# Performance work log

Measured on AMD Instinct MI355X. Metric: run time of the kernel, lower is better.

The kernel has to match this reference:

```python
import jax, jax.numpy as jnp
import numpy as np

N_NODES = 50000
N_EDGES = 800000
D_IN = 128
D_HID = 128
D_OUT = 128


def _glorot(key, shape):
    fan_in, fan_out = shape
    lim = np.sqrt(6.0 / (fan_in + fan_out))
    return jax.random.uniform(key, shape, jnp.float32, -lim, lim)


def setup_inputs() -> dict:
    key = jax.random.key(0)
    ks = jax.random.split(key, 8)
    x = jax.random.normal(ks[0], (N_NODES, D_IN), jnp.float32)
    edge_index = jax.random.randint(ks[1], (2, N_EDGES), 0, N_NODES, jnp.int64)
    # SAGEConv layer 1: lin_l (neighbor aggregate, has bias), lin_r (root, no bias)
    W1l = _glorot(ks[2], (D_IN, D_HID))
    b1 = jnp.zeros((D_HID,), jnp.float32)
    W1r = _glorot(ks[3], (D_IN, D_HID))
    # SAGEConv layer 2
    W2l = _glorot(ks[4], (D_HID, D_OUT))
    b2 = jnp.zeros((D_OUT,), jnp.float32)
    W2r = _glorot(ks[5], (D_HID, D_OUT))
    return {"x": x, "edge_index": edge_index, "W1l": W1l, "b1": b1,
            "W1r": W1r, "W2l": W2l, "b2": b2, "W2r": W2r}


def _sage_conv(x, src, dst, Wl, bl, Wr):
    # mean-aggregate neighbor features j -> i, then out = mean @ Wl + b + x @ Wr
    msg_sum = jax.ops.segment_sum(x[src], dst, num_segments=N_NODES)  # [N, F]
    cnt = jax.ops.segment_sum(jnp.ones((src.shape[0],), x.dtype), dst,
                              num_segments=N_NODES)  # [N]
    mean = msg_sum / jnp.maximum(cnt, 1.0)[:, None]
    return mean @ Wl + bl + x @ Wr


def reference(x, edge_index, W1l, b1, W1r, W2l, b2, W2r):
    src, dst = edge_index[0], edge_index[1]
    h = _sage_conv(x, src, dst, W1l, b1, W1r)
    h = jax.nn.relu(h)
    # dropout(p=0.2) is identity in eval mode
    out = _sage_conv(h, src, dst, W2l, b2, W2r)
    return out
```

## Files before the change

### kernel.cpp

```cpp
#include <hip/hip_runtime.h>

#define N_NODES 50000
#define N_EDGES 800000
#define D 128
#define CAP 64
#define NPB 512
#define NBIN 98
#define BIN_CAP 12288
#define EPB 4096

typedef __attribute__((ext_vector_type(8))) short s16x8;
typedef __attribute__((ext_vector_type(8))) unsigned short u16x8;
typedef __attribute__((ext_vector_type(4))) unsigned short u16x4;
typedef __attribute__((ext_vector_type(4))) float f32x4;

__device__ __forceinline__ unsigned short f2bf(float f) {
    unsigned u = __builtin_bit_cast(unsigned, f);
    return (unsigned short)((u + 0x7FFFu + ((u >> 16) & 1u)) >> 16);
}
__device__ __forceinline__ float bf2f(unsigned short h) {
    return __builtin_bit_cast(float, (unsigned)h << 16);
}

__device__ __forceinline__ int load_src(const int* ei, int is32, int e) {
    return is32 ? ei[e] : ei[2 * e];
}
__device__ __forceinline__ int load_dst(const int* ei, int is32, int e) {
    return is32 ? ei[N_EDGES + e] : ei[2 * N_EDGES + 2 * e];
}

__global__ void prep_kernel(const float* __restrict__ x, const int* __restrict__ ei,
                            const float* __restrict__ W1l, const float* __restrict__ W1r,
                            const float* __restrict__ W2l, const float* __restrict__ W2r,
                            unsigned short* __restrict__ xb,
                            unsigned short* __restrict__ wt1,
                            unsigned short* __restrict__ wt2,
                            int* __restrict__ flag, int* __restrict__ bin_cnt) {
    int b = blockIdx.x;
    if (b < 3125) {
        int t = b * 256 + threadIdx.x;
        float4 a = *(const float4*)(x + (size_t)t * 8);
        float4 c = *(const float4*)(x + (size_t)t * 8 + 4);
        u16x8 o;
        o[0] = f2bf(a.x); o[1] = f2bf(a.y); o[2] = f2bf(a.z); o[3] = f2bf(a.w);
        o[4] = f2bf(c.x); o[5] = f2bf(c.y); o[6] = f2bf(c.z); o[7] = f2bf(c.w);
        *(u16x8*)(xb + (size_t)t * 8) = o;
    } else if (b < 3381) {
        int idx = b - 3125;
        int layer = idx >> 7;
        int c = idx & 127;
        int k = threadIdx.x;
        const float* Wl = layer ? W2l : W1l;
        const float* Wr = layer ? W2r : W1r;
        unsigned short* wt = layer ? wt2 : wt1;
        float v = (k < 128) ? Wl[(size_t)k * 128 + c] : Wr[(size_t)(k - 128) * 128 + c];
        wt[c * 256 + k] = f2bf(v);
    } else {
        if (threadIdx.x < 128) bin_cnt[threadIdx.x] = 0;
        __shared__ int any;
        if (threadIdx.x == 0) any = 0;
        __syncthreads();
        if (ei[2 * threadIdx.x + 1] != 0) atomicOr(&any, 1);
        __syncthreads();
        if (threadIdx.x == 0) flag[0] = any;
    }
}

__global__ __launch_bounds__(256) void binp_kernel(const int* __restrict__ ei,
                                                   const int* __restrict__ flag,
                                                   int* __restrict__ bin_cnt,
                                                   unsigned* __restrict__ bins) {
    __shared__ unsigned sBuf[EPB];
    __shared__ int bcnt[128], brun[128], bpos[128], gbase[128];
    int tid = threadIdx.x;
    int blk = blockIdx.x;
    int e0 = blk * EPB + tid * 16;
    int nblk = N_EDGES - blk * EPB;
    if (nblk > EPB) nblk = EPB;
    bool valid = (tid * 16) < nblk;
    if (tid < 128) bcnt[tid] = 0;
    __syncthreads();
    unsigned packed[16];
    if (valid) {
        int is32 = flag[0];
        if (is32) {
            const int4* ps = (const int4*)(ei + e0);
            const int4* pd = (const int4*)(ei + N_EDGES + e0);
#pragma unroll
            for (int q = 0; q < 4; ++q) {
                int4 s = ps[q], d = pd[q];
                packed[q * 4 + 0] = ((unsigned)d.x << 16) | (unsigned)s.x;
                packed[q * 4 + 1] = ((unsigned)d.y << 16) | (unsigned)s.y;
                packed[q * 4 + 2] = ((unsigned)d.z << 16) | (unsigned)s.z;
                packed[q * 4 + 3] = ((unsigned)d.w << 16) | (unsigned)s.w;
            }
        } else {
            const int4* ps = (const int4*)(ei + 2 * (size_t)e0);
            const int4* pd = (const int4*)(ei + 2 * (size_t)N_EDGES + 2 * (size_t)e0);
#pragma unroll
            for (int q = 0; q < 8; ++q) {
                int4 s = ps[q], d = pd[q];
                packed[q * 2 + 0] = ((unsigned)d.x << 16) | (unsigned)s.x;
                packed[q * 2 + 1] = ((unsigned)d.z << 16) | (unsigned)s.z;
            }
        }
#pragma unroll
        for (int k = 0; k < 16; ++k) atomicAdd(&bcnt[packed[k] >> 25], 1);
    }
    __syncthreads();
    if (tid < 64) {
        int a = bcnt[2 * tid], b = bcnt[2 * tid + 1];
        int s = a + b;
        int incl = s;
#pragma unroll
        for (int o = 1; o < 64; o <<= 1) {
            int t = __shfl_up(incl, o, 64);
            if (tid >= o) incl += t;
        }
        int pref = incl - s;
        brun[2 * tid] = pref;
        brun[2 * tid + 1] = pref + a;
        bpos[2 * tid] = pref;
        bpos[2 * tid + 1] = pref + a;
    }
    __syncthreads();
    if (valid) {
#pragma unroll
        for (int k = 0; k < 16; ++k) {
            int b = packed[k] >> 25;
            int slot = atomicAdd(&bpos[b], 1);
            sBuf[slot] = packed[k];
        }
    }
    __syncthreads();
    if (tid < 128) {
        int n = bcnt[tid];
        gbase[tid] = n > 0 ? atomicAdd(&bin_cnt[tid], n) : 0;
    }
    __syncthreads();
    for (int i = tid; i < nblk; i += 256) {
        unsigned p = sBuf[i];
        int b = p >> 25;
        int gpos = gbase[b] + (i - brun[b]);
        if (gpos < BIN_CAP) bins[(size_t)b * BIN_CAP + gpos] = p;
    }
}

__global__ __launch_bounds__(256) void unbin_kernel(const int* __restrict__ bin_cnt,
                                                    const unsigned* __restrict__ bins,
                                                    int* __restrict__ cnt,
                                                    unsigned short* __restrict__ srcs16) {
    __shared__ unsigned short buck[NPB * CAP];
    __shared__ int lcnt[NPB];
    int tid = threadIdx.x;
    int bn = blockIdx.x;
    int nbase = bn * NPB;
    for (int i = tid; i < NPB; i += 256) lcnt[i] = 0;
    __syncthreads();
    int nE = bin_cnt[bn];
    if (nE > BIN_CAP) nE = BIN_CAP;
    for (int i = tid; i < nE; i += 256) {
        unsigned p = bins[(size_t)bn * BIN_CAP + i];
        int local = (int)(p >> 16) - nbase;
        if ((unsigned)local < NPB) {
            int slot = atomicAdd(&lcnt[local], 1);
            if (slot < CAP) buck[local * CAP + slot] = (unsigned short)(p & 0xFFFFu);
        }
    }
    __syncthreads();
    int nlim = N_NODES - nbase;
    if (nlim > NPB) nlim = NPB;
    const uint4* sb = (const uint4*)buck;
    uint4* go = (uint4*)(srcs16 + (size_t)nbase * CAP);
    int n4 = nlim * 8;
    for (int i = tid; i < n4; i += 256) go[i] = sb[i];
    for (int i = tid; i < nlim; i += 256) cnt[nbase + i] = lcnt[i];
}

__global__ __launch_bounds__(256) void aggp_kernel(const unsigned short* __restrict__ feat,
                                                   const int* __restrict__ cnt,
                                                   const unsigned short* __restrict__ srcs16,
                                                   unsigned short* __restrict__ agg) {
    int node = blockIdx.x * 4 + (threadIdx.x >> 6);
    if (node >= N_NODES) return;
    int lane = threadIdx.x & 63;
    int q = lane >> 4;
    int c16 = lane & 15;
    int deg = cnt[node];
    int idx = srcs16[node * CAP + lane];
    int d = deg < CAP ? deg : CAP;
    float acc[8] = {};
    for (int j = 0; j < d; j += 16) {
        int e[4];
        float m[4];
#pragma unroll
        for (int u = 0; u < 4; ++u) {
            int jj = j + u * 4 + q;
            int es = __shfl(idx, jj, 64);
            bool val = jj < d;
            e[u] = val ? es : 0;
            m[u] = val ? 1.f : 0.f;
        }
        u16x8 v[4];
#pragma unroll
        for (int u = 0; u < 4; ++u)
            v[u] = *((const u16x8*)(feat + (size_t)e[u] * D) + c16);
#pragma unroll
        for (int u = 0; u < 4; ++u)
#pragma unroll
            for (int i = 0; i < 8; ++i)
                acc[i] += bf2f((unsigned short)v[u][i]) * m[u];
    }
#pragma unroll
    for (int i = 0; i < 8; ++i) {
        acc[i] += __shfl_xor(acc[i], 16, 64);
        acc[i] += __shfl_xor(acc[i], 32, 64);
    }
    if (q == 0) {
        float s = deg > 0 ? 1.f / (float)deg : 0.f;
        u16x8 o;
#pragma unroll
        for (int i = 0; i < 8; ++i) o[i] = f2bf(acc[i] * s);
        *((u16x8*)(agg + (size_t)node * D) + c16) = o;
    }
}

template <int MODE>
__global__ __launch_bounds__(256) void mm3_kernel(const unsigned short* __restrict__ Agb,
                                                  const unsigned short* __restrict__ Rootb,
                                                  const unsigned short* __restrict__ Wt,
                                                  const float* __restrict__ bias,
                                                  float* __restrict__ C,
                                                  unsigned short* __restrict__ Cb) {
    __shared__ __align__(16) unsigned short sA[2][32][128];
    int r0 = blockIdx.x * 32;
    int tid = threadIdx.x;
    int lane = tid & 63, wid = tid >> 6;
    int l15 = lane & 15, khalf = lane >> 4;

    s16x8 bF[2][4][2];
#pragma unroll
    for (int p = 0; p < 2; ++p)
#pragma unroll
        for (int kc2 = 0; kc2 < 4; ++kc2)
#pragma unroll
            for (int nf = 0; nf < 2; ++nf) {
                int cc = wid * 32 + nf * 16 + l15;
                bF[p][kc2][nf] = *(const s16x8*)(Wt + (size_t)cc * 256 + p * 128 +
                                                 kc2 * 32 + khalf * 8);
            }

    {
        int r = tid >> 3;
        int kq = tid & 7;
        int row = r0 + r;
        u16x8 a0, a1, x0, x1;
        if (row < N_NODES) {
            const u16x8* pa = (const u16x8*)(Agb + (size_t)row * D + kq * 16);
            a0 = pa[0]; a1 = pa[1];
            const u16x8* pr = (const u16x8*)(Rootb + (size_t)row * D + kq * 16);
            x0 = pr[0]; x1 = pr[1];
        } else {
            u16x8 z = {};
            a0 = z; a1 = z; x0 = z; x1 = z;
        }
        int c0 = (kq * 2) ^ (r & 7), c1 = (kq * 2 + 1) ^ (r & 7);
        *(u16x8*)&sA[0][r][c0 * 8] = a0;
        *(u16x8*)&sA[0][r][c1 * 8] = a1;
        *(u16x8*)&sA[1][r][c0 * 8] = x0;
        *(u16x8*)&sA[1][r][c1 * 8] = x1;
    }
    __syncthreads();

    f32x4 acc[2][2] = {};
#pragma unroll
    for (int p = 0; p < 2; ++p)
#pragma unroll
        for (int kc2 = 0; kc2 < 4; ++kc2) {
            s16x8 aF[2];
#pragma unroll
            for (int mf = 0; mf < 2; ++mf) {
                int rr = mf * 16 + l15;
                int chunk = (kc2 * 4 + khalf) ^ (rr & 7);
                aF[mf] = *(const s16x8*)&sA[p][rr][chunk * 8];
            }
#pragma unroll
            for (int nf = 0; nf < 2; ++nf)
#pragma unroll
                for (int mf = 0; mf < 2; ++mf)
                    acc[mf][nf] = __builtin_amdgcn_mfma_f32_16x16x32_bf16(
                        aF[mf], bF[p][kc2][nf], acc[mf][nf], 0, 0, 0);
        }

#pragma unroll
    for (int mf = 0; mf < 2; ++mf)
#pragma unroll
        for (int nf = 0; nf < 2; ++nf) {
            int col = wid * 32 + nf * 16 + l15;
            float b = bias[col];
#pragma unroll
            for (int r = 0; r < 4; ++r) {
                int row = r0 + mf * 16 + khalf * 4 + r;
                if (row < N_NODES) {
                    float o = acc[mf][nf][r] + b;
                    if (MODE == 1) {
                        o = fmaxf(o, 0.f);
                        Cb[(size_t)row * D + col] = f2bf(o);
                    } else {
                        C[(size_t)row * D + col] = o;
                    }
                }
            }
        }
}

__global__ void initc_kernel(const int* __restrict__ ei, int* __restrict__ flag,
                             int* __restrict__ cnt) {
    int i = blockIdx.x * 256 + threadIdx.x;
    if (i < 50048) cnt[i] = 0;
    if (blockIdx.x == 0) {
        __shared__ int any;
        if (threadIdx.x == 0) any = 0;
        __syncthreads();
        if (ei[2 * threadIdx.x + 1] != 0) atomicOr(&any, 1);
        __syncthreads();
        if (threadIdx.x == 0) flag[0] = any;
    }
}

__global__ void prep_wf_kernel(const float* __restrict__ W1l, const float* __restrict__ W1r,
                               const float* __restrict__ W2l, const float* __restrict__ W2r,
                               unsigned short* __restrict__ wt1,
                               unsigned short* __restrict__ wt2) {
    int layer = blockIdx.x >> 7;
    int c = blockIdx.x & 127;
    int k = threadIdx.x;
    const float* Wl = layer ? W2l : W1l;
    const float* Wr = layer ? W2r : W1r;
    unsigned short* wt = layer ? wt2 : wt1;
    float v = (k < 128) ? Wl[(size_t)k * 128 + c] : Wr[(size_t)(k - 128) * 128 + c];
    wt[c * 256 + k] = f2bf(v);
}

__global__ void tobf_kernel(const float* __restrict__ in, unsigned short* __restrict__ out,
                            int n8) {
    int t = blockIdx.x * 256 + threadIdx.x;
    if (t >= n8) return;
    float4 a = *(const float4*)(in + (size_t)t * 8);
    float4 b = *(const float4*)(in + (size_t)t * 8 + 4);
    u16x8 o;
    o[0] = f2bf(a.x); o[1] = f2bf(a.y); o[2] = f2bf(a.z); o[3] = f2bf(a.w);
    o[4] = f2bf(b.x); o[5] = f2bf(b.y); o[6] = f2bf(b.z); o[7] = f2bf(b.w);
    *(u16x8*)(out + (size_t)t * 8) = o;
}

__global__ void hist_kernel(const int* __restrict__ ei, const int* __restrict__ flag,
                            int* __restrict__ cnt) {
    int e = blockIdx.x * blockDim.x + threadIdx.x;
    if (e >= N_EDGES) return;
    int is32 = flag[0];
    atomicAdd(&cnt[load_dst(ei, is32, e)], 1);
}

__global__ __launch_bounds__(1024) void scan_kernel(int* __restrict__ cnt_cur,
                                                    int* __restrict__ off) {
    __shared__ int wsum[16];
    __shared__ int woff[16];
    __shared__ int carry;
    __shared__ int tile_tot;
    int lane = threadIdx.x & 63;
    int wid = threadIdx.x >> 6;
    if (threadIdx.x == 0) carry = 0;
    __syncthreads();
    for (int base = 0; base < N_NODES; base += 1024) {
        int i = base + threadIdx.x;
        int v = (i < N_NODES) ? cnt_cur[i] : 0;
        int incl = v;
#pragma unroll
        for (int o = 1; o < 64; o <<= 1) {
            int t = __shfl_up(incl, o, 64);
            if (lane >= o) incl += t;
        }
        if (lane == 63) wsum[wid] = incl;
        __syncthreads();
        if (wid == 0 && lane < 16) {
            int t = wsum[lane];
            int inc2 = t;
#pragma unroll
            for (int o = 1; o < 16; o <<= 1) {
                int u = __shfl_up(inc2, o, 64);
                if (lane >= o) inc2 += u;
            }
            woff[lane] = inc2 - t;
            if (lane == 15) tile_tot = inc2;
        }
        __syncthreads();
        int c = carry;
        if (i < N_NODES) {
            int o = c + woff[wid] + (incl - v);
            off[i] = o;
            cnt_cur[i] = o;
        }
        __syncthreads();
        if (threadIdx.x == 0) carry = c + tile_tot;
        __syncthreads();
    }
    if (threadIdx.x == 0) off[N_NODES] = carry;
}

__global__ void fillc_kernel(const int* __restrict__ ei, const int* __restrict__ flag,
                             int* __restrict__ cur, int* __restrict__ srcs) {
    int e = blockIdx.x * blockDim.x + threadIdx.x;
    if (e >= N_EDGES) return;
    int is32 = flag[0];
    int d = load_dst(ei, is32, e);
    int p = atomicAdd(&cur[d], 1);
    srcs[p] = load_src(ei, is32, e);
}

__global__ __launch_bounds__(256) void aggc_kernel(const unsigned short* __restrict__ feat,
                                                   const int* __restrict__ off,
                                                   const int* __restrict__ srcs,
                                                   unsigned short* __restrict__ agg) {
    int node = blockIdx.x * 4 + (threadIdx.x >> 6);
    if (node >= N_NODES) return;
    int lane = threadIdx.x & 63;
    int half = lane >> 5;
    int c8 = lane & 31;
    int s0 = off[node], s1 = off[node + 1];
    int deg = s1 - s0;
    float a0 = 0.f, a1 = 0.f, a2 = 0.f, a3 = 0.f;
    for (int j = s0; j < s1; j += 2) {
        int jj = j + half;
        if (jj < s1) {
            int e = srcs[jj];
            u16x4 v = *((const u16x4*)(feat + (size_t)e * D) + c8);
            a0 += bf2f((unsigned short)v[0]);
            a1 += bf2f((unsigned short)v[1]);
            a2 += bf2f((unsigned short)v[2]);
            a3 += bf2f((unsigned short)v[3]);
        }
    }
    a0 += __shfl_xor(a0, 32, 64);
    a1 += __shfl_xor(a1, 32, 64);
    a2 += __shfl_xor(a2, 32, 64);
    a3 += __shfl_xor(a3, 32, 64);
    if (half == 0) {
        float s = deg > 0 ? 1.f / (float)deg : 0.f;
        u16x4 o;
        o[0] = f2bf(a0 * s); o[1] = f2bf(a1 * s);
        o[2] = f2bf(a2 * s); o[3] = f2bf(a3 * s);
        *((u16x4*)(agg + (size_t)node * D) + c8) = o;
    }
}

extern "C" void kernel_launch(void* const* d_in, const int* in_sizes, int n_in,
                              void* d_out, int out_size, void* d_ws, size_t ws_size,
                              hipStream_t stream) {
    const float* x = (const float*)d_in[0];
    const int* ei = (const int*)d_in[1];
    const float* W1l = (const float*)d_in[2];
    const float* b1 = (const float*)d_in[3];
    const float* W1r = (const float*)d_in[4];
    const float* W2l = (const float*)d_in[5];
    const float* b2 = (const float*)d_in[6];
    const float* W2r = (const float*)d_in[7];
    float* out = (float*)d_out;

    const size_t padded_need = 256 + 512 + (size_t)NBIN * BIN_CAP * 4 +
                               (size_t)50176 * CAP * 2 + 50048 * 4 + 2 * 65536 +
                               3 * (size_t)N_NODES * D * 2;

    if (ws_size >= padded_need) {
        char* w = (char*)d_ws;
        int* flag = (int*)w;                      w += 256;
        int* bin_cnt = (int*)w;                   w += 512;
        unsigned* bins = (unsigned*)w;            w += (size_t)NBIN * BIN_CAP * 4;
        unsigned short* srcs16 = (unsigned short*)w; w += (size_t)50176 * CAP * 2;
        int* cnt = (int*)w;                       w += 50048 * 4;
        unsigned short* wt1 = (unsigned short*)w; w += 65536;
        unsigned short* wt2 = (unsigned short*)w; w += 65536;
        unsigned short* xb = (unsigned short*)w;  w += (size_t)N_NODES * D * 2;
        unsigned short* hb = (unsigned short*)w;  w += (size_t)N_NODES * D * 2;
        unsigned short* aggb = (unsigned short*)w;

        prep_kernel<<<3382, 256, 0, stream>>>(x, ei, W1l, W1r, W2l, W2r, xb, wt1, wt2,
                                              flag, bin_cnt);
        binp_kernel<<<(N_EDGES + EPB - 1) / EPB, 256, 0, stream>>>(ei, flag, bin_cnt, bins);
        unbin_kernel<<<NBIN, 256, 0, stream>>>(bin_cnt, bins, cnt, srcs16);

        int nblk = (N_NODES + 31) / 32;
        aggp_kernel<<<(N_NODES + 3) / 4, 256, 0, stream>>>(xb, cnt, srcs16, aggb);
        mm3_kernel<1><<<nblk, 256, 0, stream>>>(aggb, xb, wt1, b1, nullptr, hb);

        aggp_kernel<<<(N_NODES + 3) / 4, 256, 0, stream>>>(hb, cnt, srcs16, aggb);
        mm3_kernel<2><<<nblk, 256, 0, stream>>>(aggb, hb, wt2, b2, out, nullptr);
    } else {
        char* w = (char*)d_ws;
        int* flag = (int*)w;                      w += 256;
        int* cur = (int*)w;                       w += 50048 * 4;
        int* off = (int*)w;                       w += 50056 * 4;
        int* srcs = (int*)w;                      w += (size_t)N_EDGES * 4;
        unsigned short* wt1 = (unsigned short*)w; w += 65536;
        unsigned short* wt2 = (unsigned short*)w; w += 65536;
        unsigned short* xb = (unsigned short*)w;  w += (size_t)N_NODES * D * 2;
        unsigned short* aggb = (unsigned short*)w;

        initc_kernel<<<196, 256, 0, stream>>>(ei, flag, cur);
        prep_wf_kernel<<<256, 256, 0, stream>>>(W1l, W1r, W2l, W2r, wt1, wt2);
        tobf_kernel<<<(N_NODES * D / 8 + 255) / 256, 256, 0, stream>>>(x, xb, N_NODES * D / 8);
        hist_kernel<<<(N_EDGES + 255) / 256, 256, 0, stream>>>(ei, flag, cur);
        scan_kernel<<<1, 1024, 0, stream>>>(cur, off);
        fillc_kernel<<<(N_EDGES + 255) / 256, 256, 0, stream>>>(ei, flag, cur, srcs);

        int nblk = (N_NODES + 31) / 32;
        aggc_kernel<<<(N_NODES + 3) / 4, 256, 0, stream>>>(xb, off, srcs, aggb);
        mm3_kernel<1><<<nblk, 256, 0, stream>>>(aggb, xb, wt1, b1, nullptr, xb);

        aggc_kernel<<<(N_NODES + 3) / 4, 256, 0, stream>>>(xb, off, srcs, aggb);
        mm3_kernel<2><<<nblk, 256, 0, stream>>>(aggb, xb, wt2, b2, out, nullptr);
    }
}
```

Before: 127.0 us.

## Fuse mean aggregation with the dual GEMM in one kernel per layer

Replaces the separate aggregation kernel and MFMA GEMM kernel with one fused kernel per SAGE layer. Each 512-thread block gathers neighbor means for its 32 rows straight into shared memory, loads the root rows, then runs the MFMA with each wave covering 16 output columns. This removes the aggregated-feature round trip through global memory and two launches. In exchange each wave now handles 4 nodes serially, and there are fewer, larger blocks for the gather phase, which could reduce latency hiding.

```diff
diff --git a/kernel.cpp b/kernel.cpp
--- a/kernel.cpp
+++ b/kernel.cpp
@@ -177,102 +177,90 @@
     for (int i = tid; i < nlim; i += 256) cnt[nbase + i] = lcnt[i];
 }
 
-__global__ __launch_bounds__(256) void aggp_kernel(const unsigned short* __restrict__ feat,
-                                                   const int* __restrict__ cnt,
-                                                   const unsigned short* __restrict__ srcs16,
-                                                   unsigned short* __restrict__ agg) {
-    int node = blockIdx.x * 4 + (threadIdx.x >> 6);
-    if (node >= N_NODES) return;
-    int lane = threadIdx.x & 63;
-    int q = lane >> 4;
-    int c16 = lane & 15;
-    int deg = cnt[node];
-    int idx = srcs16[node * CAP + lane];
-    int d = deg < CAP ? deg : CAP;
-    float acc[8] = {};
-    for (int j = 0; j < d; j += 16) {
-        int e[4];
-        float m[4];
-#pragma unroll
-        for (int u = 0; u < 4; ++u) {
-            int jj = j + u * 4 + q;
-            int es = __shfl(idx, jj, 64);
-            bool val = jj < d;
-            e[u] = val ? es : 0;
-            m[u] = val ? 1.f : 0.f;
-        }
-        u16x8 v[4];
-#pragma unroll
-        for (int u = 0; u < 4; ++u)
-            v[u] = *((const u16x8*)(feat + (size_t)e[u] * D) + c16);
-#pragma unroll
-        for (int u = 0; u < 4; ++u)
-#pragma unroll
-            for (int i = 0; i < 8; ++i)
-                acc[i] += bf2f((unsigned short)v[u][i]) * m[u];
-    }
-#pragma unroll
-    for (int i = 0; i < 8; ++i) {
-        acc[i] += __shfl_xor(acc[i], 16, 64);
-        acc[i] += __shfl_xor(acc[i], 32, 64);
-    }
-    if (q == 0) {
-        float s = deg > 0 ? 1.f / (float)deg : 0.f;
-        u16x8 o;
-#pragma unroll
-        for (int i = 0; i < 8; ++i) o[i] = f2bf(acc[i] * s);
-        *((u16x8*)(agg + (size_t)node * D) + c16) = o;
-    }
-}
-
 template <int MODE>
-__global__ __launch_bounds__(256) void mm3_kernel(const unsigned short* __restrict__ Agb,
-                                                  const unsigned short* __restrict__ Rootb,
-                                                  const unsigned short* __restrict__ Wt,
-                                                  const float* __restrict__ bias,
-                                                  float* __restrict__ C,
-                                                  unsigned short* __restrict__ Cb) {
+__global__ __launch_bounds__(512, 4) void fused_kernel(
+    const unsigned short* __restrict__ feat,
+    const int* __restrict__ cnt,
+    const unsigned short* __restrict__ srcs16,
+    const unsigned short* __restrict__ Wt,
+    const float* __restrict__ bias,
+    float* __restrict__ C, unsigned short* __restrict__ Cb) {
     __shared__ __align__(16) unsigned short sA[2][32][128];
     int r0 = blockIdx.x * 32;
     int tid = threadIdx.x;
     int lane = tid & 63, wid = tid >> 6;
     int l15 = lane & 15, khalf = lane >> 4;
 
-    s16x8 bF[2][4][2];
+    int rr_ = tid >> 4, rkq = tid & 15;
+    int rowX = r0 + rr_;
+    u16x8 vroot = {};
+    if (rowX < N_NODES)
+        vroot = *(const u16x8*)(feat + (size_t)rowX * D + rkq * 8);
+
+    s16x8 bF[2][4];
 #pragma unroll
     for (int p = 0; p < 2; ++p)
 #pragma unroll
         for (int kc2 = 0; kc2 < 4; ++kc2)
-#pragma unroll
-            for (int nf = 0; nf < 2; ++nf) {
-                int cc = wid * 32 + nf * 16 + l15;
-                bF[p][kc2][nf] = *(const s16x8*)(Wt + (size_t)cc * 256 + p * 128 +
-                                                 kc2 * 32 + khalf * 8);
-            }
+            bF[p][kc2] = *(const s16x8*)(Wt + (size_t)(wid * 16 + l15) * 256 +
+                                         p * 128 + kc2 * 32 + khalf * 8);
 
     {
-        int r = tid >> 3;
-        int kq = tid & 7;
-        int row = r0 + r;
-        u16x8 a0, a1, x0, x1;
-        if (row < N_NODES) {
-            const u16x8* pa = (const u16x8*)(Agb + (size_t)row * D + kq * 16);
-            a0 = pa[0]; a1 = pa[1];
-            const u16x8* pr = (const u16x8*)(Rootb + (size_t)row * D + kq * 16);
-            x0 = pr[0]; x1 = pr[1];
-        } else {
-            u16x8 z = {};
-            a0 = z; a1 = z; x0 = z; x1 = z;
-        }
-        int c0 = (kq * 2) ^ (r & 7), c1 = (kq * 2 + 1) ^ (r & 7);
-        *(u16x8*)&sA[0][r][c0 * 8] = a0;
-        *(u16x8*)&sA[0][r][c1 * 8] = a1;
-        *(u16x8*)&sA[1][r][c0 * 8] = x0;
-        *(u16x8*)&sA[1][r][c1 * 8] = x1;
-    }
-    __syncthreads();
-
-    f32x4 acc[2][2] = {};
+        int nb = r0 + wid * 4;
+        int q = lane >> 4, c16 = lane & 15;
+        int4 d4 = *(const int4*)(cnt + nb);
+        int degs[4] = {d4.x, d4.y, d4.z, d4.w};
+        int idxA[4];
+#pragma unroll
+        for (int k = 0; k < 4; ++k)
+            idxA[k] = srcs16[(size_t)(nb + k) * CAP + lane];
+#pragma unroll
+        for (int k = 0; k < 4; ++k) {
+            int node = nb + k;
+            int deg = (node < N_NODES) ? degs[k] : 0;
+            int dd = deg < CAP ? deg : CAP;
+            float acc[8] = {};
+            for (int j = 0; j < dd; j += 16) {
+                int e[4];
+                float m[4];
+#pragma unroll
+                for (int u = 0; u < 4; ++u) {
+                    int jj = j + u * 4 + q;
+                    int es = __shfl(idxA[k], jj, 64);
+                    bool val = jj < dd;
+                    e[u] = val ? es : 0;
+                    m[u] = val ? 1.f : 0.f;
+                }
+                u16x8 v[4];
+#pragma unroll
+                for (int u = 0; u < 4; ++u)
+                    v[u] = *((const u16x8*)(feat + (size_t)e[u] * D) + c16);
+#pragma unroll
+                for (int u = 0; u < 4; ++u)
+#pragma unroll
+                    for (int i = 0; i < 8; ++i)
+                        acc[i] += bf2f((unsigned short)v[u][i]) * m[u];
+            }
+#pragma unroll
+            for (int i = 0; i < 8; ++i) {
+                acc[i] += __shfl_xor(acc[i], 16, 64);
+                acc[i] += __shfl_xor(acc[i], 32, 64);
+            }
+            if (q == 0 && node < N_NODES) {
+                float s = deg > 0 ? 1.f / (float)deg : 0.f;
+                u16x8 o;
+#pragma unroll
+                for (int i = 0; i < 8; ++i) o[i] = f2bf(acc[i] * s);
+                int lr = wid * 4 + k;
+                *(u16x8*)&sA[0][lr][(c16 ^ (lr & 7)) * 8] = o;
+            }
+        }
+    }
+
+    *(u16x8*)&sA[1][rr_][(rkq ^ (rr_ & 7)) * 8] = vroot;
+    __syncthreads();
+
+    f32x4 acc2[2] = {};
 #pragma unroll
     for (int p = 0; p < 2; ++p)
 #pragma unroll
@@ -285,24 +273,21 @@
                 aF[mf] = *(const s16x8*)&sA[p][rr][chunk * 8];
             }
 #pragma unroll
-            for (int nf = 0; nf < 2; ++nf)
-#pragma unroll
-                for (int mf = 0; mf < 2; ++mf)
-                    acc[mf][nf] = __builtin_amdgcn_mfma_f32_16x16x32_bf16(
-                        aF[mf], bF[p][kc2][nf], acc[mf][nf], 0, 0, 0);
-        }
-
-#pragma unroll
-    for (int mf = 0; mf < 2; ++mf)
-#pragma unroll
-        for (int nf = 0; nf < 2; ++nf) {
-            int col = wid * 32 + nf * 16 + l15;
-            float b = bias[col];
+            for (int mf = 0; mf < 2; ++mf)
+                acc2[mf] = __builtin_amdgcn_mfma_f32_16x16x32_bf16(
+                    aF[mf], bF[p][kc2], acc2[mf], 0, 0, 0);
+        }
+
+    {
+        int col = wid * 16 + l15;
+        float b = bias[col];
+#pragma unroll
+        for (int mf = 0; mf < 2; ++mf)
 #pragma unroll
             for (int r = 0; r < 4; ++r) {
                 int row = r0 + mf * 16 + khalf * 4 + r;
                 if (row < N_NODES) {
-                    float o = acc[mf][nf][r] + b;
+                    float o = acc2[mf][r] + b;
                     if (MODE == 1) {
                         o = fmaxf(o, 0.f);
                         Cb[(size_t)row * D + col] = f2bf(o);
@@ -311,7 +296,7 @@
                     }
                 }
             }
-        }
+    }
 }
 
 __global__ void initc_kernel(const int* __restrict__ ei, int* __restrict__ flag,
@@ -454,6 +439,94 @@
     }
 }
 
+template <int MODE>
+__global__ __launch_bounds__(256) void mm3_kernel(const unsigned short* __restrict__ Agb,
+                                                  const unsigned short* __restrict__ Rootb,
+                                                  const unsigned short* __restrict__ Wt,
+                                                  const float* __restrict__ bias,
+                                                  float* __restrict__ C,
+                                                  unsigned short* __restrict__ Cb) {
+    __shared__ __align__(16) unsigned short sA[2][32][128];
+    int r0 = blockIdx.x * 32;
+    int tid = threadIdx.x;
+    int lane = tid & 63, wid = tid >> 6;
+    int l15 = lane & 15, khalf = lane >> 4;
+
+    s16x8 bF[2][4][2];
+#pragma unroll
+    for (int p = 0; p < 2; ++p)
+#pragma unroll
+        for (int kc2 = 0; kc2 < 4; ++kc2)
+#pragma unroll
+            for (int nf = 0; nf < 2; ++nf) {
+                int cc = wid * 32 + nf * 16 + l15;
+                bF[p][kc2][nf] = *(const s16x8*)(Wt + (size_t)cc * 256 + p * 128 +
+                                                 kc2 * 32 + khalf * 8);
+            }
+    {
+        int r = tid >> 3;
+        int kq = tid & 7;
+        int row = r0 + r;
+        u16x8 a0, a1, x0, x1;
+        if (row < N_NODES) {
+            const u16x8* pa = (const u16x8*)(Agb + (size_t)row * D + kq * 16);
+            a0 = pa[0]; a1 = pa[1];
+            const u16x8* pr = (const u16x8*)(Rootb + (size_t)row * D + kq * 16);
+            x0 = pr[0]; x1 = pr[1];
+        } else {
+            u16x8 z = {};
+            a0 = z; a1 = z; x0 = z; x1 = z;
+        }
+        int c0 = (kq * 2) ^ (r & 7), c1 = (kq * 2 + 1) ^ (r & 7);
+        *(u16x8*)&sA[0][r][c0 * 8] = a0;
+        *(u16x8*)&sA[0][r][c1 * 8] = a1;
+        *(u16x8*)&sA[1][r][c0 * 8] = x0;
+        *(u16x8*)&sA[1][r][c1 * 8] = x1;
+    }
+    __syncthreads();
+
+    f32x4 acc[2][2] = {};
+#pragma unroll
+    for (int p = 0; p < 2; ++p)
+#pragma unroll
+        for (int kc2 = 0; kc2 < 4; ++kc2) {
+            s16x8 aF[2];
+#pragma unroll
+            for (int mf = 0; mf < 2; ++mf) {
+                int rr = mf * 16 + l15;
+                int chunk = (kc2 * 4 + khalf) ^ (rr & 7);
+                aF[mf] = *(const s16x8*)&sA[p][rr][chunk * 8];
+            }
+#pragma unroll
+            for (int nf = 0; nf < 2; ++nf)
+#pragma unroll
+                for (int mf = 0; mf < 2; ++mf)
+                    acc[mf][nf] = __builtin_amdgcn_mfma_f32_16x16x32_bf16(
+                        aF[mf], bF[p][kc2][nf], acc[mf][nf], 0, 0, 0);
+        }
+
+#pragma unroll
+    for (int mf = 0; mf < 2; ++mf)
+#pragma unroll
+        for (int nf = 0; nf < 2; ++nf) {
+            int col = wid * 32 + nf * 16 + l15;
+            float b = bias[col];
+#pragma unroll
+            for (int r = 0; r < 4; ++r) {
+                int row = r0 + mf * 16 + khalf * 4 + r;
+                if (row < N_NODES) {
+                    float o = acc[mf][nf][r] + b;
+                    if (MODE == 1) {
+                        o = fmaxf(o, 0.f);
+                        Cb[(size_t)row * D + col] = f2bf(o);
+                    } else {
+                        C[(size_t)row * D + col] = o;
+                    }
+                }
+            }
+        }
+}
+
 extern "C" void kernel_launch(void* const* d_in, const int* in_sizes, int n_in,
                               void* d_out, int out_size, void* d_ws, size_t ws_size,
                               hipStream_t stream) {
@@ -469,7 +542,7 @@
 
     const size_t padded_need = 256 + 512 + (size_t)NBIN * BIN_CAP * 4 +
                                (size_t)50176 * CAP * 2 + 50048 * 4 + 2 * 65536 +
-                               3 * (size_t)N_NODES * D * 2;
+                               2 * (size_t)N_NODES * D * 2;
 
     if (ws_size >= padded_need) {
         char* w = (char*)d_ws;
@@ -481,8 +554,7 @@
         unsigned short* wt1 = (unsigned short*)w; w += 65536;
         unsigned short* wt2 = (unsigned short*)w; w += 65536;
         unsigned short* xb = (unsigned short*)w;  w += (size_t)N_NODES * D * 2;
-        unsigned short* hb = (unsigned short*)w;  w += (size_t)N_NODES * D * 2;
-        unsigned short* aggb = (unsigned short*)w;
+        unsigned short* hb = (unsigned short*)w;
 
         prep_kernel<<<3382, 256, 0, stream>>>(x, ei, W1l, W1r, W2l, W2r, xb, wt1, wt2,
                                               flag, bin_cnt);
@@ -490,11 +562,8 @@
         unbin_kernel<<<NBIN, 256, 0, stream>>>(bin_cnt, bins, cnt, srcs16);
 
         int nblk = (N_NODES + 31) / 32;
-        aggp_kernel<<<(N_NODES + 3) / 4, 256, 0, stream>>>(xb, cnt, srcs16, aggb);
-        mm3_kernel<1><<<nblk, 256, 0, stream>>>(aggb, xb, wt1, b1, nullptr, hb);
-
-        aggp_kernel<<<(N_NODES + 3) / 4, 256, 0, stream>>>(hb, cnt, srcs16, aggb);
-        mm3_kernel<2><<<nblk, 256, 0, stream>>>(aggb, hb, wt2, b2, out, nullptr);
+        fused_kernel<1><<<nblk, 512, 0, stream>>>(xb, cnt, srcs16, wt1, b1, nullptr, hb);
+        fused_kernel<2><<<nblk, 512, 0, stream>>>(hb, cnt, srcs16, wt2, b2, out, nullptr);
     } else {
         char* w = (char*)d_ws;
         int* flag = (int*)w;                      w += 256;
```

New measurement: 126.5 us. No clear change (-0.4%).

## Fuse prep and binning kernels, unroll aggregation gather, alias hidden buffers

Applied to the files above, without the earlier changes.

Merges the conversion/weight-transpose kernel with the edge-binning kernel into one launch. Each binning block now recomputes the int32/int64 format flag locally, and the bin counters are zeroed with a memset. The aggregation kernel replaces its 16-edge loop with a fixed 32-edge unrolled gather plus an optional second 32-edge batch, aiming for more loads in flight. Buffers are reused in place: the layer-1 matmul writes its output over xb, which removes one N×D workspace. The cost is extra masked gathers for low-degree nodes, and the in-place write depends on each matmul block reading its rows before it writes them.

```diff
diff --git a/kernel.cpp b/kernel.cpp
--- a/kernel.cpp
+++ b/kernel.cpp
@@ -29,60 +29,53 @@
     return is32 ? ei[N_EDGES + e] : ei[2 * N_EDGES + 2 * e];
 }
 
-__global__ void prep_kernel(const float* __restrict__ x, const int* __restrict__ ei,
-                            const float* __restrict__ W1l, const float* __restrict__ W1r,
-                            const float* __restrict__ W2l, const float* __restrict__ W2r,
-                            unsigned short* __restrict__ xb,
-                            unsigned short* __restrict__ wt1,
-                            unsigned short* __restrict__ wt2,
-                            int* __restrict__ flag, int* __restrict__ bin_cnt) {
+__global__ __launch_bounds__(256) void prepbin_kernel(
+    const float* __restrict__ x, const int* __restrict__ ei,
+    const float* __restrict__ W1l, const float* __restrict__ W1r,
+    const float* __restrict__ W2l, const float* __restrict__ W2r,
+    unsigned short* __restrict__ xb, unsigned short* __restrict__ wt1,
+    unsigned short* __restrict__ wt2, int* __restrict__ bin_cnt,
+    unsigned* __restrict__ bins) {
+    __shared__ unsigned sBuf[EPB];
+    __shared__ int bcnt[128], brun[128], bpos[128], gbase[128];
+    __shared__ int sAny;
     int b = blockIdx.x;
+    int tid = threadIdx.x;
     if (b < 3125) {
-        int t = b * 256 + threadIdx.x;
+        int t = b * 256 + tid;
         float4 a = *(const float4*)(x + (size_t)t * 8);
         float4 c = *(const float4*)(x + (size_t)t * 8 + 4);
         u16x8 o;
         o[0] = f2bf(a.x); o[1] = f2bf(a.y); o[2] = f2bf(a.z); o[3] = f2bf(a.w);
         o[4] = f2bf(c.x); o[5] = f2bf(c.y); o[6] = f2bf(c.z); o[7] = f2bf(c.w);
         *(u16x8*)(xb + (size_t)t * 8) = o;
-    } else if (b < 3381) {
+        return;
+    }
+    if (b < 3381) {
         int idx = b - 3125;
         int layer = idx >> 7;
         int c = idx & 127;
-        int k = threadIdx.x;
         const float* Wl = layer ? W2l : W1l;
         const float* Wr = layer ? W2r : W1r;
         unsigned short* wt = layer ? wt2 : wt1;
-        float v = (k < 128) ? Wl[(size_t)k * 128 + c] : Wr[(size_t)(k - 128) * 128 + c];
-        wt[c * 256 + k] = f2bf(v);
-    } else {
-        if (threadIdx.x < 128) bin_cnt[threadIdx.x] = 0;
-        __shared__ int any;
-        if (threadIdx.x == 0) any = 0;
-        __syncthreads();
-        if (ei[2 * threadIdx.x + 1] != 0) atomicOr(&any, 1);
-        __syncthreads();
-        if (threadIdx.x == 0) flag[0] = any;
-    }
-}
-
-__global__ __launch_bounds__(256) void binp_kernel(const int* __restrict__ ei,
-                                                   const int* __restrict__ flag,
-                                                   int* __restrict__ bin_cnt,
-                                                   unsigned* __restrict__ bins) {
-    __shared__ unsigned sBuf[EPB];
-    __shared__ int bcnt[128], brun[128], bpos[128], gbase[128];
-    int tid = threadIdx.x;
-    int blk = blockIdx.x;
+        float v = (tid < 128) ? Wl[(size_t)tid * 128 + c]
+                              : Wr[(size_t)(tid - 128) * 128 + c];
+        wt[c * 256 + tid] = f2bf(v);
+        return;
+    }
+    int blk = b - 3381;
     int e0 = blk * EPB + tid * 16;
     int nblk = N_EDGES - blk * EPB;
     if (nblk > EPB) nblk = EPB;
     bool valid = (tid * 16) < nblk;
+    if (tid == 0) sAny = 0;
     if (tid < 128) bcnt[tid] = 0;
     __syncthreads();
+    if (ei[2 * tid + 1] != 0) atomicOr(&sAny, 1);
+    __syncthreads();
+    int is32 = sAny;
     unsigned packed[16];
     if (valid) {
-        int is32 = flag[0];
         if (is32) {
             const int4* ps = (const int4*)(ei + e0);
             const int4* pd = (const int4*)(ei + N_EDGES + e0);
@@ -109,8 +102,8 @@
     }
     __syncthreads();
     if (tid < 64) {
-        int a = bcnt[2 * tid], b = bcnt[2 * tid + 1];
-        int s = a + b;
+        int a = bcnt[2 * tid], bb = bcnt[2 * tid + 1];
+        int s = a + bb;
         int incl = s;
 #pragma unroll
         for (int o = 1; o < 64; o <<= 1) {
@@ -127,8 +120,8 @@
     if (valid) {
 #pragma unroll
         for (int k = 0; k < 16; ++k) {
-            int b = packed[k] >> 25;
-            int slot = atomicAdd(&bpos[b], 1);
+            int bin = packed[k] >> 25;
+            int slot = atomicAdd(&bpos[bin], 1);
             sBuf[slot] = packed[k];
         }
     }
@@ -140,9 +133,9 @@
     __syncthreads();
     for (int i = tid; i < nblk; i += 256) {
         unsigned p = sBuf[i];
-        int b = p >> 25;
-        int gpos = gbase[b] + (i - brun[b]);
-        if (gpos < BIN_CAP) bins[(size_t)b * BIN_CAP + gpos] = p;
+        int bin = p >> 25;
+        int gpos = gbase[bin] + (i - brun[bin]);
+        if (gpos < BIN_CAP) bins[(size_t)bin * BIN_CAP + gpos] = p;
     }
 }
 
@@ -187,26 +180,47 @@
     int q = lane >> 4;
     int c16 = lane & 15;
     int deg = cnt[node];
-    int idx = srcs16[node * CAP + lane];
+    int idx = srcs16[(size_t)node * CAP + lane];
     int d = deg < CAP ? deg : CAP;
     float acc[8] = {};
-    for (int j = 0; j < d; j += 16) {
-        int e[4];
-        float m[4];
-#pragma unroll
-        for (int u = 0; u < 4; ++u) {
-            int jj = j + u * 4 + q;
+    {
+        int e[8];
+        float m[8];
+#pragma unroll
+        for (int u = 0; u < 8; ++u) {
+            int jj = u * 4 + q;
             int es = __shfl(idx, jj, 64);
             bool val = jj < d;
             e[u] = val ? es : 0;
             m[u] = val ? 1.f : 0.f;
         }
-        u16x8 v[4];
-#pragma unroll
-        for (int u = 0; u < 4; ++u)
+        u16x8 v[8];
+#pragma unroll
+        for (int u = 0; u < 8; ++u)
             v[u] = *((const u16x8*)(feat + (size_t)e[u] * D) + c16);
 #pragma unroll
-        for (int u = 0; u < 4; ++u)
+        for (int u = 0; u < 8; ++u)
+#pragma unroll
+            for (int i = 0; i < 8; ++i)
+                acc[i] += bf2f((unsigned short)v[u][i]) * m[u];
+    }
+    if (d > 32) {
+        int e[8];
+        float m[8];
+#pragma unroll
+        for (int u = 0; u < 8; ++u) {
+            int jj = 32 + u * 4 + q;
+            int es = __shfl(idx, jj, 64);
+            bool val = jj < d;
+            e[u] = val ? es : 0;
+            m[u] = val ? 1.f : 0.f;
+        }
+        u16x8 v[8];
+#pragma unroll
+        for (int u = 0; u < 8; ++u)
+            v[u] = *((const u16x8*)(feat + (size_t)e[u] * D) + c16);
+#pragma unroll
+        for (int u = 0; u < 8; ++u)
 #pragma unroll
             for (int i = 0; i < 8; ++i)
                 acc[i] += bf2f((unsigned short)v[u][i]) * m[u];
@@ -249,7 +263,6 @@
                 bF[p][kc2][nf] = *(const s16x8*)(Wt + (size_t)cc * 256 + p * 128 +
                                                  kc2 * 32 + khalf * 8);
             }
-
     {
         int r = tid >> 3;
         int kq = tid & 7;
@@ -467,13 +480,12 @@
     const float* W2r = (const float*)d_in[7];
     float* out = (float*)d_out;
 
-    const size_t padded_need = 256 + 512 + (size_t)NBIN * BIN_CAP * 4 +
+    const size_t padded_need = 512 + (size_t)NBIN * BIN_CAP * 4 +
                                (size_t)50176 * CAP * 2 + 50048 * 4 + 2 * 65536 +
-                               3 * (size_t)N_NODES * D * 2;
+                               2 * (size_t)N_NODES * D * 2;
 
     if (ws_size >= padded_need) {
         char* w = (char*)d_ws;
-        int* flag = (int*)w;                      w += 256;
         int* bin_cnt = (int*)w;                   w += 512;
         unsigned* bins = (unsigned*)w;            w += (size_t)NBIN * BIN_CAP * 4;
         unsigned short* srcs16 = (unsigned short*)w; w += (size_t)50176 * CAP * 2;
@@ -481,20 +493,19 @@
         unsigned short* wt1 = (unsigned short*)w; w += 65536;
         unsigned short* wt2 = (unsigned short*)w; w += 65536;
         unsigned short* xb = (unsigned short*)w;  w += (size_t)N_NODES * D * 2;
-        unsigned short* hb = (unsigned short*)w;  w += (size_t)N_NODES * D * 2;
-        unsigned short* aggb = (unsigned short*)w;
-
-        prep_kernel<<<3382, 256, 0, stream>>>(x, ei, W1l, W1r, W2l, W2r, xb, wt1, wt2,
-                                              flag, bin_cnt);
-        binp_kernel<<<(N_EDGES + EPB - 1) / EPB, 256, 0, stream>>>(ei, flag, bin_cnt, bins);
+        unsigned short* hb = (unsigned short*)w;
+
+        hipMemsetAsync(bin_cnt, 0, 512, stream);
+        prepbin_kernel<<<3577, 256, 0, stream>>>(x, ei, W1l, W1r, W2l, W2r, xb, wt1,
+                                                 wt2, bin_cnt, bins);
         unbin_kernel<<<NBIN, 256, 0, stream>>>(bin_cnt, bins, cnt, srcs16);
 
         int nblk = (N_NODES + 31) / 32;
-        aggp_kernel<<<(N_NODES + 3) / 4, 256, 0, stream>>>(xb, cnt, srcs16, aggb);
-        mm3_kernel<1><<<nblk, 256, 0, stream>>>(aggb, xb, wt1, b1, nullptr, hb);
-
-        aggp_kernel<<<(N_NODES + 3) / 4, 256, 0, stream>>>(hb, cnt, srcs16, aggb);
-        mm3_kernel<2><<<nblk, 256, 0, stream>>>(aggb, hb, wt2, b2, out, nullptr);
+        aggp_kernel<<<(N_NODES + 3) / 4, 256, 0, stream>>>(xb, cnt, srcs16, hb);
+        mm3_kernel<1><<<nblk, 256, 0, stream>>>(hb, xb, wt1, b1, nullptr, xb);
+
+        aggp_kernel<<<(N_NODES + 3) / 4, 256, 0, stream>>>(xb, cnt, srcs16, hb);
+        mm3_kernel<2><<<nblk, 256, 0, stream>>>(hb, xb, wt2, b2, out, nullptr);
     } else {
         char* w = (char*)d_ws;
         int* flag = (int*)w;                      w += 256;
```

New measurement: 134.7 us. 6.0% more time.
